# Kernel optimization log

Measured on AMD Instinct MI355X. Metric: run time of the kernel, lower is better.

Reference implementation:

```python
import jax, jax.numpy as jnp
import numpy as np

H = W = D = 128   # output volume resolution
GS = 3            # control grid size per axis
N = GS * GS * GS  # 27 control points
B = 2


def _build_constants():
    # Sampling grid: matches np.meshgrid(linspace(w), linspace(h), linspace(d)) in __init__
    gX, gY, gZ = np.meshgrid(np.linspace(-1, 1, W), np.linspace(-1, 1, H), np.linspace(-1, 1, D))
    grid = np.stack([gX, gY, gZ], axis=-1).astype(np.float32)  # (H,W,D,3)
    # Control points: P_Y, P_X, P_Z = np.meshgrid(ax, ax, ax), reshaped (-1,1)
    ax = np.linspace(-1, 1, GS)
    P_Y, P_X, P_Z = np.meshgrid(ax, ax, ax)
    P = np.stack([P_X.reshape(-1), P_Y.reshape(-1), P_Z.reshape(-1)], axis=1).astype(np.float32)  # (N,3)
    # TPS L matrix and its inverse (compute_L_inverse)
    d2 = ((P[:, None, :] - P[None, :, :]) ** 2).sum(-1)
    d2[d2 == 0] = 1.0
    K = d2 * np.log(d2)
    Pm = np.concatenate([np.ones((N, 1), np.float32), P], axis=1)  # (N,4)
    L = np.zeros((N + 4, N + 4), np.float64)
    L[:N, :N] = K
    L[:N, N:] = Pm
    L[N:, :N] = Pm.T
    Li = np.linalg.inv(L).astype(np.float32)  # (N+4, N+4)
    return grid, P, Li


def setup_inputs() -> dict:
    key = jax.random.key(0)
    grid, P, Li = _build_constants()
    theta = jax.random.normal(key, (B, 3 * N), dtype=jnp.float32)
    return {"theta": theta, "grid": jnp.asarray(grid), "P": jnp.asarray(P), "Li": jnp.asarray(Li)}


def reference(theta, grid, P, Li):
    b = theta.shape[0]
    n = P.shape[0]
    # theta[:, :N]=Q_X, theta[:, N:2N]=Q_Y, theta[:, 2N:]=Q_Z -> (B,3,N)
    Q = theta.reshape(b, 3, n)
    Wc = jnp.einsum('nm,bcm->bcn', Li[:n, :n], Q)   # (B,3,N) RBF weights
    Ac = jnp.einsum('am,bcm->bca', Li[n:, :n], Q)   # (B,3,4) affine part
    # Squared distances from every grid point to every control point: (H,W,D,N)
    dx = grid[..., 0, None] - P[:, 0]
    dy = grid[..., 1, None] - P[:, 1]
    dz = grid[..., 2, None] - P[:, 2]
    r2 = dx * dx + dy * dy + dz * dz
    r2 = jnp.where(r2 == 0, 1.0, r2)
    U = r2 * jnp.log(r2)  # TPS kernel r^2 log r^2, (H,W,D,N)
    nonlin = jnp.einsum('hwdn,bcn->bhwdc', U, Wc)               # (B,H,W,D,3)
    affine = Ac[:, None, None, None, :, 0] + jnp.einsum('hwda,bca->bhwdc', grid, Ac[:, :, 1:])
    return affine + nonlin  # (B,H,W,D,3) warped grid
```

## Files before the change

### kernel.cpp

```cpp
#include <hip/hip_runtime.h>
#include <math.h>


#define NP 27
#define NV 31

__global__ __launch_bounds__(192) void tps_prep(
    const float* __restrict__ theta,
    const float* __restrict__ Li,
    float* __restrict__ V)
{
    int t = threadIdx.x;
    if (t >= 6 * NV) return;
    int bc = t / NV;
    int k  = t % NV;
    const float* q  = theta + bc * NP;
    const float* lr = Li + k * NV;
    float acc = 0.f;
    #pragma unroll
    for (int m = 0; m < NP; ++m) acc = fmaf(lr[m], q[m], acc);
    if (k < NP) acc *= 0.69314718055994531f;
    V[t] = acc;
}

__global__ __launch_bounds__(256) void tps_main(
    const float* __restrict__ V,
    float* __restrict__ out)
{
    const int idx = blockIdx.x * 256 + threadIdx.x;
    const int d = idx & 127;
    const int w = (idx >> 7) & 127;
    const int h = idx >> 14;

    const float s = 1.0f / 127.0f;
    const float gx = (float)(2 * w - 127) * s;
    const float gy = (float)(2 * h - 127) * s;
    const float gz = (float)(2 * d - 127) * s;

    float ex[3], ey[3], ez[3];
    ex[0] = (gx + 1.f) * (gx + 1.f); ex[1] = gx * gx; ex[2] = (gx - 1.f) * (gx - 1.f);
    ey[0] = (gy + 1.f) * (gy + 1.f); ey[1] = gy * gy; ey[2] = (gy - 1.f) * (gy - 1.f);
    ez[0] = (gz + 1.f) * (gz + 1.f); ez[1] = gz * gz; ez[2] = (gz - 1.f) * (gz - 1.f);

    float U[NP + 1];
    #pragma unroll
    for (int i = 0; i < 3; ++i) {
        #pragma unroll
        for (int j = 0; j < 3; ++j) {
            const float exy = ex[i] + ey[j];
            #pragma unroll
            for (int k = 0; k < 3; ++k) {
                float r2 = exy + ez[k];
                r2 = fmaxf(r2, 1e-37f);
                U[i * 9 + j * 3 + k] = r2 * __log2f(r2);
            }
        }
    }
    U[NP] = 1.0f;

    const int HWD = 1 << 21;
    #pragma unroll
    for (int b = 0; b < 2; ++b) {
        float o[3];
        #pragma unroll
        for (int c = 0; c < 3; ++c) {
            const float* v = V + (b * 3 + c) * NV;
            float acc = gx * v[NP + 1];
            acc = fmaf(gy, v[NP + 2], acc);
            acc = fmaf(gz, v[NP + 3], acc);
            #pragma unroll
            for (int n = 0; n < NP + 1; ++n) acc = fmaf(U[n], v[n], acc);
            o[c] = acc;
        }
        float* op = out + ((size_t)(b * HWD + idx)) * 3;
        op[0] = o[0]; op[1] = o[1]; op[2] = o[2];
    }
}

extern "C" void kernel_launch(void* const* d_in, const int* in_sizes, int n_in,
                              void* d_out, int out_size, void* d_ws, size_t ws_size,
                              hipStream_t stream) {
    const float* theta = (const float*)d_in[0];
    const float* Li    = (const float*)d_in[3];
    float* V   = (float*)d_ws;
    float* out = (float*)d_out;

    tps_prep<<<1, 192, 0, stream>>>(theta, Li, V);
    tps_main<<<(1 << 21) / 256, 256, 0, stream>>>(V, out);
}
```

Before: 100.9 us.

## Process four voxels per thread with float4 stores and constant-address coefficient loads

Each thread now computes four consecutive depth voxels, reusing the x/y distance terms and writing its 12 outputs as three float4 stores instead of scalar strided stores. The coefficient table is padded to 32 floats per row and read through the constant address space so the loads can become scalar loads. Launch bounds request three blocks per CU. The trade-off is four times fewer threads, higher register pressure from holding 4x28 kernel values, and fewer waves available to hide store latency.

```diff
diff --git a/kernel.cpp b/kernel.cpp
--- a/kernel.cpp
+++ b/kernel.cpp
@@ -3,7 +3,9 @@
 
 
 #define NP 27
-#define NV 31
+#define RS 32
+
+typedef const __attribute__((address_space(4))) float* cfp;
 
 __global__ __launch_bounds__(192) void tps_prep(
     const float* __restrict__ theta,
@@ -11,69 +13,83 @@
     float* __restrict__ V)
 {
     int t = threadIdx.x;
-    if (t >= 6 * NV) return;
-    int bc = t / NV;
-    int k  = t % NV;
-    const float* q  = theta + bc * NP;
-    const float* lr = Li + k * NV;
+    int bc = t >> 5;
+    int k  = t & 31;
     float acc = 0.f;
-    #pragma unroll
-    for (int m = 0; m < NP; ++m) acc = fmaf(lr[m], q[m], acc);
-    if (k < NP) acc *= 0.69314718055994531f;
-    V[t] = acc;
+    if (k < 31) {
+        const float* q  = theta + bc * NP;
+        const float* lr = Li + k * 31;
+        #pragma unroll
+        for (int m = 0; m < NP; ++m) acc = fmaf(lr[m], q[m], acc);
+        if (k < NP) acc *= 0.69314718055994531f;
+    }
+    V[bc * RS + k] = acc;
 }
 
-__global__ __launch_bounds__(256) void tps_main(
-    const float* __restrict__ V,
+__global__ __launch_bounds__(256, 3) void tps_main(
+    const float* __restrict__ Vg,
     float* __restrict__ out)
 {
-    const int idx = blockIdx.x * 256 + threadIdx.x;
-    const int d = idx & 127;
-    const int w = (idx >> 7) & 127;
-    const int h = idx >> 14;
+    cfp V = (cfp)(unsigned long long)Vg;
+
+    const int t = blockIdx.x * 256 + threadIdx.x;
+    const int idx0 = t << 2;
+    const int d0 = idx0 & 127;
+    const int w  = (idx0 >> 7) & 127;
+    const int h  = idx0 >> 14;
 
     const float s = 1.0f / 127.0f;
     const float gx = (float)(2 * w - 127) * s;
     const float gy = (float)(2 * h - 127) * s;
-    const float gz = (float)(2 * d - 127) * s;
 
-    float ex[3], ey[3], ez[3];
+    float ex[3], ey[3];
     ex[0] = (gx + 1.f) * (gx + 1.f); ex[1] = gx * gx; ex[2] = (gx - 1.f) * (gx - 1.f);
     ey[0] = (gy + 1.f) * (gy + 1.f); ey[1] = gy * gy; ey[2] = (gy - 1.f) * (gy - 1.f);
-    ez[0] = (gz + 1.f) * (gz + 1.f); ez[1] = gz * gz; ez[2] = (gz - 1.f) * (gz - 1.f);
 
-    float U[NP + 1];
+    float U[4][NP + 1];
+    float gz[4];
     #pragma unroll
-    for (int i = 0; i < 3; ++i) {
+    for (int p = 0; p < 4; ++p) {
+        gz[p] = (float)(2 * (d0 + p) - 127) * s;
+        float ez[3];
+        ez[0] = (gz[p] + 1.f) * (gz[p] + 1.f);
+        ez[1] = gz[p] * gz[p];
+        ez[2] = (gz[p] - 1.f) * (gz[p] - 1.f);
         #pragma unroll
-        for (int j = 0; j < 3; ++j) {
-            const float exy = ex[i] + ey[j];
+        for (int i = 0; i < 3; ++i) {
             #pragma unroll
-            for (int k = 0; k < 3; ++k) {
-                float r2 = exy + ez[k];
-                r2 = fmaxf(r2, 1e-37f);
-                U[i * 9 + j * 3 + k] = r2 * __log2f(r2);
+            for (int j = 0; j < 3; ++j) {
+                const float exy = ex[i] + ey[j];
+                #pragma unroll
+                for (int k = 0; k < 3; ++k) {
+                    float r2 = exy + ez[k];
+                    r2 = fmaxf(r2, 1e-37f);
+                    U[p][i * 9 + j * 3 + k] = r2 * __log2f(r2);
+                }
             }
         }
+        U[p][NP] = 1.0f;
     }
-    U[NP] = 1.0f;
 
     const int HWD = 1 << 21;
     #pragma unroll
     for (int b = 0; b < 2; ++b) {
-        float o[3];
+        float o[4][3];
         #pragma unroll
         for (int c = 0; c < 3; ++c) {
-            const float* v = V + (b * 3 + c) * NV;
-            float acc = gx * v[NP + 1];
-            acc = fmaf(gy, v[NP + 2], acc);
-            acc = fmaf(gz, v[NP + 3], acc);
+            cfp v = V + (b * 3 + c) * RS;
             #pragma unroll
-            for (int n = 0; n < NP + 1; ++n) acc = fmaf(U[n], v[n], acc);
-            o[c] = acc;
+            for (int p = 0; p < 4; ++p) {
+                float a = fmaf(gx, v[NP + 1], fmaf(gy, v[NP + 2], gz[p] * v[NP + 3]));
+                #pragma unroll
+                for (int n = 0; n < NP + 1; ++n) a = fmaf(U[p][n], v[n], a);
+                o[p][c] = a;
+            }
         }
-        float* op = out + ((size_t)(b * HWD + idx)) * 3;
-        op[0] = o[0]; op[1] = o[1]; op[2] = o[2];
+        float4* op = (float4*)(out + ((size_t)(b * HWD + idx0)) * 3);
+        op[0] = make_float4(o[0][0], o[0][1], o[0][2], o[1][0]);
+        op[1] = make_float4(o[1][1], o[1][2], o[2][0], o[2][1]);
+        op[2] = make_float4(o[2][2], o[3][0], o[3][1], o[3][2]);
     }
 }
 
@@ -86,5 +102,5 @@
     float* out = (float*)d_out;
 
     tps_prep<<<1, 192, 0, stream>>>(theta, Li, V);
-    tps_main<<<(1 << 21) / 256, 256, 0, stream>>>(V, out);
+    tps_main<<<(1 << 21) / (4 * 256), 256, 0, stream>>>(V, out);
 }
```

Result: no change. 101.5 us (+0.6%).
